# Kernel tuning notes

Measured on AMD Instinct MI355X. Metric: run time of the kernel, lower is better.

The kernel has to match this reference:

```python
import jax, jax.numpy as jnp
import numpy as np

NUM_LAYERS = 3
DROPOUT_P = 0.1


def _spmm(rows, cols, vals, X, num_rows):
    # COO SpMM: out[r] = sum_{e: rows[e]==r} vals[e] * X[cols[e]]
    return jax.ops.segment_sum(vals[:, None] * X[cols], rows, num_segments=num_rows)


def setup_inputs() -> dict:
    key = jax.random.key(0)
    ks = jax.random.split(key, 8)
    N, H, D, NNZ = 50000, 50000, 256, 1600000
    poi_embs = jax.random.normal(ks[0], (N, D), dtype=jnp.float32)
    src_row = jax.random.randint(ks[1], (NNZ,), 0, N, dtype=jnp.int32)
    src_col = jax.random.randint(ks[2], (NNZ,), 0, H, dtype=jnp.int32)
    src_val = jax.random.uniform(ks[3], (NNZ,), dtype=jnp.float32)
    tar_row = jax.random.randint(ks[4], (NNZ,), 0, H, dtype=jnp.int32)
    tar_col = jax.random.randint(ks[5], (NNZ,), 0, N, dtype=jnp.int32)
    tar_val = jax.random.uniform(ks[6], (NNZ,), dtype=jnp.float32)
    return {
        "poi_embs": poi_embs,
        "src_row": src_row, "src_col": src_col, "src_val": src_val,
        "tar_row": tar_row, "tar_col": tar_col, "tar_val": tar_val,
        "num_pois": N, "num_hyperedges": H,
    }


def reference(poi_embs, src_row, src_col, src_val, tar_row, tar_col, tar_val,
              num_pois, num_hyperedges):
    keep = 1.0 - DROPOUT_P
    drop_key = jax.random.key(42)
    finals = [poi_embs]  # [N, D]
    x = poi_embs
    for i in range(NUM_LAYERS):
        msg_tar = _spmm(tar_row, tar_col, tar_val, x, num_hyperedges)   # [H, D]
        msg_src = _spmm(src_row, src_col, src_val, msg_tar, num_pois)   # [N, D]
        h = msg_src + finals[-1]
        mask = jax.random.bernoulli(jax.random.fold_in(drop_key, i), keep, h.shape)
        x = jnp.where(mask, h / keep, 0.0)  # inverted dropout, training=True
        finals.append(x)
    return jnp.mean(jnp.stack(finals), axis=0)
```

## Files before the change

kernel.cpp:

```cpp
#include <hip/hip_runtime.h>
#include <hip/hip_fp16.h>
#include <stdint.h>

#define DD 256
#define BK_SHIFT 10
#define NB 98
#define CHUNK 4096

typedef float    fx4 __attribute__((ext_vector_type(4)));
typedef uint32_t ux2 __attribute__((ext_vector_type(2)));

__host__ __device__ __forceinline__ uint32_t rotl32(uint32_t v, int r) {
  return (v << r) | (v >> (32 - r));
}

__host__ __device__ inline void tf2x32(uint32_t k0, uint32_t k1,
                                       uint32_t& x0, uint32_t& x1) {
  uint32_t ks0 = k0, ks1 = k1, ks2 = k0 ^ k1 ^ 0x1BD11BDAu;
  x0 += ks0; x1 += ks1;
#define TF_RND(r) { x0 += x1; x1 = rotl32(x1, (r)); x1 ^= x0; }
  TF_RND(13) TF_RND(15) TF_RND(26) TF_RND(6)
  x0 += ks1; x1 += ks2 + 1u;
  TF_RND(17) TF_RND(29) TF_RND(16) TF_RND(24)
  x0 += ks2; x1 += ks0 + 2u;
  TF_RND(13) TF_RND(15) TF_RND(26) TF_RND(6)
  x0 += ks0; x1 += ks1 + 3u;
  TF_RND(17) TF_RND(29) TF_RND(16) TF_RND(24)
  x0 += ks1; x1 += ks2 + 4u;
  TF_RND(13) TF_RND(15) TF_RND(26) TF_RND(6)
  x0 += ks2; x1 += ks0 + 5u;
#undef TF_RND
}

__device__ __forceinline__ float2 h2f(uint32_t u) {
  __half2 h = *(__half2*)&u;
  return __half22float2(h);
}

__global__ void init_kernel(const float* __restrict__ p, uint32_t* __restrict__ xh,
                            int total4) {
  int t4 = blockIdx.x * blockDim.x + threadIdx.x;
  if (t4 >= total4) return;
  fx4 v = __builtin_nontemporal_load((const fx4*)p + t4);
  __half2 h0 = __floats2half2_rn(v.x, v.y);
  __half2 h1 = __floats2half2_rn(v.z, v.w);
  ux2 u;
  u.x = *(const uint32_t*)&h0;
  u.y = *(const uint32_t*)&h1;
  __builtin_nontemporal_store(u, (ux2*)xh + t4);
}

__global__ __launch_bounds__(256) void bucket_hist(
    const int* __restrict__ t_row, int nnz_t,
    const int* __restrict__ s_row, int nnz_s,
    int* __restrict__ gbcnt, int H) {
  __shared__ int lcnt[NB];
  for (int i = threadIdx.x; i < NB; i += 256) lcnt[i] = 0;
  __syncthreads();
  const int base = blockIdx.x * CHUNK;
  const int nnz_all = nnz_t + nnz_s;
#pragma unroll
  for (int k = 0; k < CHUNK / 256; ++k) {
    int e = base + k * 256 + threadIdx.x;
    if (e < nnz_all) {
      int slot = (e < nnz_t) ? t_row[e] : (H + s_row[e - nnz_t]);
      atomicAdd(&lcnt[slot >> BK_SHIFT], 1);
    }
  }
  __syncthreads();
  for (int i = threadIdx.x; i < NB; i += 256)
    if (lcnt[i]) atomicAdd(&gbcnt[i], lcnt[i]);
}

__global__ void bucket_scan(const int* __restrict__ gbcnt,
                            int* __restrict__ bbase, int* __restrict__ gcur) {
  if (threadIdx.x == 0) {
    int run = 0;
    for (int i = 0; i < NB; ++i) { bbase[i] = run; gcur[i] = run; run += gbcnt[i]; }
    bbase[NB] = run;
  }
}

__global__ __launch_bounds__(256) void coarse_scatter(
    const int* __restrict__ t_row, const int* __restrict__ t_col,
    const float* __restrict__ t_val, int nnz_t,
    const int* __restrict__ s_row, const int* __restrict__ s_col,
    const float* __restrict__ s_val, int nnz_s,
    int* __restrict__ gcur, uint64_t* __restrict__ staging, int H) {
  __shared__ int lcnt[NB], lbase[NB], gofs[NB];
  __shared__ int ltotal;
  __shared__ uint64_t stage[CHUNK];
  const int tid = threadIdx.x;
  for (int i = tid; i < NB; i += 256) lcnt[i] = 0;
  __syncthreads();
  const int base = blockIdx.x * CHUNK;
  const int nnz_all = nnz_t + nnz_s;
  uint64_t rec[CHUNK / 256];
#pragma unroll
  for (int k = 0; k < CHUNK / 256; ++k) {
    int e = base + k * 256 + tid;
    if (e < nnz_all) {
      int slot, col; float val;
      if (e < nnz_t) { slot = t_row[e]; col = t_col[e]; val = t_val[e]; }
      else { int i2 = e - nnz_t; slot = H + s_row[i2]; col = s_col[i2]; val = s_val[i2]; }
      uint32_t packed = ((uint32_t)col << 16) |
                        (uint32_t)__half_as_ushort(__float2half_rn(val));
      rec[k] = ((uint64_t)(uint32_t)slot << 32) | packed;
      atomicAdd(&lcnt[slot >> BK_SHIFT], 1);
    } else {
      rec[k] = ~0ull;
    }
  }
  __syncthreads();
  if (tid == 0) {
    int run = 0;
    for (int i = 0; i < NB; ++i) { lbase[i] = run; run += lcnt[i]; }
    ltotal = run;
  }
  __syncthreads();
  if (tid < NB) {
    if (lcnt[tid]) gofs[tid] = atomicAdd(&gcur[tid], lcnt[tid]);
    lcnt[tid] = 0;
  }
  __syncthreads();
#pragma unroll
  for (int k = 0; k < CHUNK / 256; ++k) {
    int slot = (int)(rec[k] >> 32);
    if (slot >= 0) {
      int b = slot >> BK_SHIFT;
      int p = atomicAdd(&lcnt[b], 1);
      stage[lbase[b] + p] = rec[k];
    }
  }
  __syncthreads();
  const int tot = ltotal;
  for (int i = tid; i < tot; i += 256) {
    uint64_t r = stage[i];
    int b = (int)(r >> 32) >> BK_SHIFT;
    staging[(size_t)gofs[b] + (i - lbase[b])] = r;
  }
}

__global__ __launch_bounds__(256) void fine_scatter(
    const uint64_t* __restrict__ staging, const int* __restrict__ bbase,
    int* __restrict__ offs, uint32_t* __restrict__ epk, int slots) {
  __shared__ int scnt[1024];
  __shared__ int sofs[1024];
  __shared__ int wsum[4];
  const int b = blockIdx.x;
  const int bb = bbase[b], be = bbase[b + 1];
  const int tid = threadIdx.x;
  for (int i = tid; i < 1024; i += 256) scnt[i] = 0;
  __syncthreads();
  for (int i = bb + tid; i < be; i += 256)
    atomicAdd(&scnt[(int)(staging[i] >> 32) & 1023], 1);
  __syncthreads();
  const int base4 = tid * 4;
  int v[4], pre[4];
#pragma unroll
  for (int k = 0; k < 4; ++k) v[k] = scnt[base4 + k];
  int tsum = 0;
#pragma unroll
  for (int k = 0; k < 4; ++k) { pre[k] = tsum; tsum += v[k]; }
  int lane = tid & 63, wv = tid >> 6;
  int inc = tsum;
  for (int off = 1; off < 64; off <<= 1) {
    int up = __shfl_up(inc, off, 64);
    if (lane >= off) inc += up;
  }
  if (lane == 63) wsum[wv] = inc;
  __syncthreads();
  int wbase = 0;
  for (int w = 0; w < wv; ++w) wbase += wsum[w];
  int texc = wbase + inc - tsum;
#pragma unroll
  for (int k = 0; k < 4; ++k) sofs[base4 + k] = texc + pre[k];
  __syncthreads();
#pragma unroll
  for (int k = 0; k < 4; ++k) {
    int g = (b << BK_SHIFT) + base4 + k;
    if (g < slots) offs[g] = bb + sofs[base4 + k] + v[k];
  }
  __syncthreads();
  for (int i = bb + tid; i < be; i += 256) {
    uint64_t r = staging[i];
    int ls = (int)(r >> 32) & 1023;
    int p = atomicAdd(&sofs[ls], 1);
    epk[(size_t)bb + p] = (uint32_t)r;
  }
}

#define GATHER_BODY(SRC)                                                          \
  float4 acc = make_float4(0.f, 0.f, 0.f, 0.f);                                   \
  int i = b;                                                                      \
  for (; i + 7 < e; i += 8) {                                                     \
    uint32_t E[8]; uint2 A[8];                                                    \
    _Pragma("unroll")                                                             \
    for (int k = 0; k < 8; ++k) E[k] = __builtin_nontemporal_load(ep + i + k);    \
    _Pragma("unroll")                                                             \
    for (int k = 0; k < 8; ++k) A[k] = SRC[(size_t)(E[k] >> 16) * 64 + lane];     \
    _Pragma("unroll")                                                             \
    for (int k = 0; k < 8; ++k) {                                                 \
      float v = __half2float(__ushort_as_half((unsigned short)(E[k] & 0xFFFFu))); \
      float2 f0 = h2f(A[k].x), f1 = h2f(A[k].y);                                  \
      acc.x += v * f0.x; acc.y += v * f0.y;                                       \
      acc.z += v * f1.x; acc.w += v * f1.y;                                       \
    }                                                                             \
  }                                                                               \
  for (; i < e; ++i) {                                                            \
    uint32_t E0 = __builtin_nontemporal_load(ep + i);                             \
    uint2 A0 = SRC[(size_t)(E0 >> 16) * 64 + lane];                               \
    float v = __half2float(__ushort_as_half((unsigned short)(E0 & 0xFFFFu)));     \
    float2 f0 = h2f(A0.x), f1 = h2f(A0.y);                                        \
    acc.x += v * f0.x; acc.y += v * f0.y;                                         \
    acc.z += v * f1.x; acc.w += v * f1.y;                                         \
  }

__global__ __launch_bounds__(256) void spmm_full(
    const int* __restrict__ offs, const uint32_t* __restrict__ ep,
    const uint2* __restrict__ X, uint2* __restrict__ Y, int nrows, int grow_base) {
  int wid = threadIdx.x >> 6, lane = threadIdx.x & 63;
  int r = blockIdx.x * 4 + wid;
  if (r >= nrows) return;
  int g = grow_base + r;
  int b = (g == 0) ? 0 : offs[g - 1];
  int e = offs[g];
  GATHER_BODY(X)
  __half2 o0 = __floats2half2_rn(acc.x, acc.y);
  __half2 o1 = __floats2half2_rn(acc.z, acc.w);
  uint2 o;
  o.x = *(const uint32_t*)&o0;
  o.y = *(const uint32_t*)&o1;
  Y[(size_t)r * 64 + lane] = o;
}

__global__ __launch_bounds__(256) void spmm_drop(
    const int* __restrict__ offs, const uint32_t* __restrict__ ep,
    const uint2* __restrict__ T, const uint2* __restrict__ xprev,
    uint2* __restrict__ xout, uint32_t k0, uint32_t k1, int nrows, int grow_base) {
  int wid = threadIdx.x >> 6, lane = threadIdx.x & 63;
  int r = blockIdx.x * 4 + wid;
  if (r >= nrows) return;
  int g = grow_base + r;
  int b = (g == 0) ? 0 : offs[g - 1];
  int e = offs[g];
  GATHER_BODY(T)
  size_t xi = (size_t)r * 64 + lane;
  ux2 xv_u = __builtin_nontemporal_load((const ux2*)xprev + xi);
  float2 x0f = h2f(xv_u.x), x1f = h2f(xv_u.y);
  float h[4] = {acc.x + x0f.x, acc.y + x0f.y, acc.z + x1f.x, acc.w + x1f.y};
  int j0 = r * DD + lane * 4;
  float xn[4];
#pragma unroll
  for (int k = 0; k < 4; ++k) {
    uint32_t r0 = 0u, r1 = (uint32_t)(j0 + k);
    tf2x32(k0, k1, r0, r1);
    uint32_t bits = r0 ^ r1;
    float u = __uint_as_float((bits >> 9) | 0x3f800000u) - 1.0f;
    xn[k] = (u < 0.9f) ? h[k] * (1.0f / 0.9f) : 0.0f;
  }
  __half2 nx0 = __floats2half2_rn(xn[0], xn[1]);
  __half2 nx1 = __floats2half2_rn(xn[2], xn[3]);
  ux2 nxu;
  nxu.x = *(const uint32_t*)&nx0;
  nxu.y = *(const uint32_t*)&nx1;
  __builtin_nontemporal_store(nxu, (ux2*)xout + xi);
}

__global__ __launch_bounds__(256) void spmm_drop_final(
    const int* __restrict__ offs, const uint32_t* __restrict__ ep,
    const uint2* __restrict__ T, const uint2* __restrict__ x0,
    const uint2* __restrict__ x1, const uint2* __restrict__ x2,
    float* __restrict__ out, uint32_t k0, uint32_t k1, int nrows, int grow_base) {
  int wid = threadIdx.x >> 6, lane = threadIdx.x & 63;
  int r = blockIdx.x * 4 + wid;
  if (r >= nrows) return;
  int g = grow_base + r;
  int b = (g == 0) ? 0 : offs[g - 1];
  int e = offs[g];
  GATHER_BODY(T)
  size_t xi = (size_t)r * 64 + lane;
  ux2 x2u = __builtin_nontemporal_load((const ux2*)x2 + xi);
  float2 q0 = h2f(x2u.x), q1 = h2f(x2u.y);
  float h[4] = {acc.x + q0.x, acc.y + q0.y, acc.z + q1.x, acc.w + q1.y};
  int j0 = r * DD + lane * 4;
  float xn[4];
#pragma unroll
  for (int k = 0; k < 4; ++k) {
    uint32_t r0 = 0u, r1 = (uint32_t)(j0 + k);
    tf2x32(k0, k1, r0, r1);
    uint32_t bits = r0 ^ r1;
    float u = __uint_as_float((bits >> 9) | 0x3f800000u) - 1.0f;
    xn[k] = (u < 0.9f) ? h[k] * (1.0f / 0.9f) : 0.0f;
  }
  ux2 x0u = __builtin_nontemporal_load((const ux2*)x0 + xi);
  ux2 x1u = __builtin_nontemporal_load((const ux2*)x1 + xi);
  float2 p0 = h2f(x0u.x), p1 = h2f(x0u.y);
  float2 a0 = h2f(x1u.x), a1 = h2f(x1u.y);
  fx4 ov;
  ov.x = 0.25f * (p0.x + a0.x + q0.x + xn[0]);
  ov.y = 0.25f * (p0.y + a0.y + q0.y + xn[1]);
  ov.z = 0.25f * (p1.x + a1.x + q1.x + xn[2]);
  ov.w = 0.25f * (p1.y + a1.y + q1.y + xn[3]);
  __builtin_nontemporal_store(ov, (fx4*)out + xi);
}

extern "C" void kernel_launch(void* const* d_in, const int* in_sizes, int n_in,
                              void* d_out, int out_size, void* d_ws, size_t ws_size,
                              hipStream_t stream) {
  const float* p     = (const float*)d_in[0];
  const int*   s_row = (const int*)d_in[1];
  const int*   s_col = (const int*)d_in[2];
  const float* s_val = (const float*)d_in[3];
  const int*   t_row = (const int*)d_in[4];
  const int*   t_col = (const int*)d_in[5];
  const float* t_val = (const float*)d_in[6];

  const int nnz_s = in_sizes[1];
  const int nnz_t = in_sizes[4];
  const int N = in_sizes[0] / DD;
  const int H = 50000;
  const int slots = H + N;
  const int nnz_all = nnz_t + nnz_s;

  uint2*    x0      = (uint2*)d_ws;
  uint2*    x1      = x0 + (size_t)N * 64;
  uint2*    th      = x1 + (size_t)N * 64;
  uint64_t* staging = (uint64_t*)(th + (size_t)H * 64);
  uint2*    x2      = (uint2*)staging;
  uint32_t* epk     = (uint32_t*)(staging + nnz_all);
  int*      offs    = (int*)(epk + nnz_all);
  int*      gbcnt   = offs + slots;
  int*      bbase   = gbcnt + NB;
  int*      gcur    = bbase + (NB + 1);

  float* out = (float*)d_out;

  (void)hipMemsetAsync(gbcnt, 0, sizeof(int) * NB, stream);
  const int cblocks = (nnz_all + CHUNK - 1) / CHUNK;
  bucket_hist<<<cblocks, 256, 0, stream>>>(t_row, nnz_t, s_row, nnz_s, gbcnt, H);
  bucket_scan<<<1, 64, 0, stream>>>(gbcnt, bbase, gcur);
  coarse_scatter<<<cblocks, 256, 0, stream>>>(t_row, t_col, t_val, nnz_t,
                                              s_row, s_col, s_val, nnz_s,
                                              gcur, staging, H);
  fine_scatter<<<NB, 256, 0, stream>>>(staging, bbase, offs, epk, slots);

  const int total4 = N * DD / 4;
  init_kernel<<<(total4 + 255) / 256, 256, 0, stream>>>(p, (uint32_t*)x0, total4);

  uint32_t key[3][2];
  for (int i = 0; i < 3; ++i) {
    uint32_t a = 0u, b = (uint32_t)i;
    tf2x32(0u, 42u, a, b);
    key[i][0] = a; key[i][1] = b;
  }

  spmm_full<<<(H + 3) / 4, 256, 0, stream>>>(offs, epk, x0, th, H, 0);
  spmm_drop<<<(N + 3) / 4, 256, 0, stream>>>(offs, epk, th, x0, x1,
                                             key[0][0], key[0][1], N, H);
  spmm_full<<<(H + 3) / 4, 256, 0, stream>>>(offs, epk, x1, th, H, 0);
  spmm_drop<<<(N + 3) / 4, 256, 0, stream>>>(offs, epk, th, x1, x2,
                                             key[1][0], key[1][1], N, H);
  spmm_full<<<(H + 3) / 4, 256, 0, stream>>>(offs, epk, x2, th, H, 0);
  spmm_drop_final<<<(N + 3) / 4, 256, 0, stream>>>(offs, epk, th, x0, x1, x2, out,
                                                   key[2][0], key[2][1], N, H);
}
```

Baseline: 815.1 us.

## Replace bucket histogram pass with fixed-slack bucket regions; unroll gather by 16

```diff
diff --git a/kernel.cpp b/kernel.cpp
--- a/kernel.cpp
+++ b/kernel.cpp
@@ -4,7 +4,9 @@
 
 #define DD 256
 #define BK_SHIFT 10
+#define BK_MASK 1023
 #define NB 98
+#define SLACK 40960
 #define CHUNK 4096
 
 typedef float    fx4 __attribute__((ext_vector_type(4)));
@@ -50,35 +52,9 @@
   __builtin_nontemporal_store(u, (ux2*)xh + t4);
 }
 
-__global__ __launch_bounds__(256) void bucket_hist(
-    const int* __restrict__ t_row, int nnz_t,
-    const int* __restrict__ s_row, int nnz_s,
-    int* __restrict__ gbcnt, int H) {
-  __shared__ int lcnt[NB];
-  for (int i = threadIdx.x; i < NB; i += 256) lcnt[i] = 0;
-  __syncthreads();
-  const int base = blockIdx.x * CHUNK;
-  const int nnz_all = nnz_t + nnz_s;
-#pragma unroll
-  for (int k = 0; k < CHUNK / 256; ++k) {
-    int e = base + k * 256 + threadIdx.x;
-    if (e < nnz_all) {
-      int slot = (e < nnz_t) ? t_row[e] : (H + s_row[e - nnz_t]);
-      atomicAdd(&lcnt[slot >> BK_SHIFT], 1);
-    }
-  }
-  __syncthreads();
-  for (int i = threadIdx.x; i < NB; i += 256)
-    if (lcnt[i]) atomicAdd(&gbcnt[i], lcnt[i]);
-}
-
-__global__ void bucket_scan(const int* __restrict__ gbcnt,
-                            int* __restrict__ bbase, int* __restrict__ gcur) {
-  if (threadIdx.x == 0) {
-    int run = 0;
-    for (int i = 0; i < NB; ++i) { bbase[i] = run; gcur[i] = run; run += gbcnt[i]; }
-    bbase[NB] = run;
-  }
+__global__ void gcur_init(int* __restrict__ gcur) {
+  int i = blockIdx.x * blockDim.x + threadIdx.x;
+  if (i < NB) gcur[i] = i * SLACK;
 }
 
 __global__ __launch_bounds__(256) void coarse_scatter(
@@ -142,18 +118,19 @@
 }
 
 __global__ __launch_bounds__(256) void fine_scatter(
-    const uint64_t* __restrict__ staging, const int* __restrict__ bbase,
+    const uint64_t* __restrict__ staging, const int* __restrict__ gcur,
     int* __restrict__ offs, uint32_t* __restrict__ epk, int slots) {
   __shared__ int scnt[1024];
   __shared__ int sofs[1024];
   __shared__ int wsum[4];
   const int b = blockIdx.x;
-  const int bb = bbase[b], be = bbase[b + 1];
+  const int bb = b * SLACK;
+  const int be = gcur[b];
   const int tid = threadIdx.x;
   for (int i = tid; i < 1024; i += 256) scnt[i] = 0;
   __syncthreads();
   for (int i = bb + tid; i < be; i += 256)
-    atomicAdd(&scnt[(int)(staging[i] >> 32) & 1023], 1);
+    atomicAdd(&scnt[(int)(staging[i] >> 32) & BK_MASK], 1);
   __syncthreads();
   const int base4 = tid * 4;
   int v[4], pre[4];
@@ -184,37 +161,46 @@
   __syncthreads();
   for (int i = bb + tid; i < be; i += 256) {
     uint64_t r = staging[i];
-    int ls = (int)(r >> 32) & 1023;
+    int ls = (int)(r >> 32) & BK_MASK;
     int p = atomicAdd(&sofs[ls], 1);
     epk[(size_t)bb + p] = (uint32_t)r;
   }
 }
 
-#define GATHER_BODY(SRC)                                                          \
-  float4 acc = make_float4(0.f, 0.f, 0.f, 0.f);                                   \
-  int i = b;                                                                      \
-  for (; i + 7 < e; i += 8) {                                                     \
-    uint32_t E[8]; uint2 A[8];                                                    \
+#define GB_STEP(NN)                                                               \
+  for (; i + (NN - 1) < e; i += NN) {                                             \
+    uint32_t E[NN]; uint2 A[NN];                                                  \
     _Pragma("unroll")                                                             \
-    for (int k = 0; k < 8; ++k) E[k] = __builtin_nontemporal_load(ep + i + k);    \
+    for (int k = 0; k < NN; ++k) E[k] = __builtin_nontemporal_load(ep + i + k);   \
     _Pragma("unroll")                                                             \
-    for (int k = 0; k < 8; ++k) A[k] = SRC[(size_t)(E[k] >> 16) * 64 + lane];     \
+    for (int k = 0; k < NN; ++k) A[k] = SRC_PTR[(size_t)(E[k] >> 16) * 64 + lane];\
     _Pragma("unroll")                                                             \
-    for (int k = 0; k < 8; ++k) {                                                 \
+    for (int k = 0; k < NN; ++k) {                                                \
       float v = __half2float(__ushort_as_half((unsigned short)(E[k] & 0xFFFFu))); \
       float2 f0 = h2f(A[k].x), f1 = h2f(A[k].y);                                  \
       acc.x += v * f0.x; acc.y += v * f0.y;                                       \
       acc.z += v * f1.x; acc.w += v * f1.y;                                       \
     }                                                                             \
-  }                                                                               \
+  }
+
+#define GATHER_BODY(SRC)                                                          \
+  float4 acc = make_float4(0.f, 0.f, 0.f, 0.f);                                   \
+  const uint2* SRC_PTR = (SRC);                                                   \
+  int i = b;                                                                      \
+  GB_STEP(16)                                                                     \
+  GB_STEP(8)                                                                      \
   for (; i < e; ++i) {                                                            \
     uint32_t E0 = __builtin_nontemporal_load(ep + i);                             \
-    uint2 A0 = SRC[(size_t)(E0 >> 16) * 64 + lane];                               \
+    uint2 A0 = SRC_PTR[(size_t)(E0 >> 16) * 64 + lane];                           \
     float v = __half2float(__ushort_as_half((unsigned short)(E0 & 0xFFFFu)));     \
     float2 f0 = h2f(A0.x), f1 = h2f(A0.y);                                        \
     acc.x += v * f0.x; acc.y += v * f0.y;                                         \
     acc.z += v * f1.x; acc.w += v * f1.y;                                         \
   }
+
+#define ROW_BOUNDS(G)                                                             \
+  int b = ((G) & BK_MASK) ? offs[(G) - 1] : ((G) >> BK_SHIFT) * SLACK;            \
+  int e = offs[(G)];
 
 __global__ __launch_bounds__(256) void spmm_full(
     const int* __restrict__ offs, const uint32_t* __restrict__ ep,
@@ -223,8 +209,7 @@
   int r = blockIdx.x * 4 + wid;
   if (r >= nrows) return;
   int g = grow_base + r;
-  int b = (g == 0) ? 0 : offs[g - 1];
-  int e = offs[g];
+  ROW_BOUNDS(g)
   GATHER_BODY(X)
   __half2 o0 = __floats2half2_rn(acc.x, acc.y);
   __half2 o1 = __floats2half2_rn(acc.z, acc.w);
@@ -242,8 +227,7 @@
   int r = blockIdx.x * 4 + wid;
   if (r >= nrows) return;
   int g = grow_base + r;
-  int b = (g == 0) ? 0 : offs[g - 1];
-  int e = offs[g];
+  ROW_BOUNDS(g)
   GATHER_BODY(T)
   size_t xi = (size_t)r * 64 + lane;
   ux2 xv_u = __builtin_nontemporal_load((const ux2*)xprev + xi);
@@ -276,8 +260,7 @@
   int r = blockIdx.x * 4 + wid;
   if (r >= nrows) return;
   int g = grow_base + r;
-  int b = (g == 0) ? 0 : offs[g - 1];
-  int e = offs[g];
+  ROW_BOUNDS(g)
   GATHER_BODY(T)
   size_t xi = (size_t)r * 64 + lane;
   ux2 x2u = __builtin_nontemporal_load((const ux2*)x2 + xi);
@@ -324,26 +307,22 @@
   const int nnz_all = nnz_t + nnz_s;
 
   uint2*    x0      = (uint2*)d_ws;
-  uint2*    x1      = x0 + (size_t)N * 64;
-  uint2*    th      = x1 + (size_t)N * 64;
-  uint64_t* staging = (uint64_t*)(th + (size_t)H * 64);
-  uint2*    x2      = (uint2*)staging;
-  uint32_t* epk     = (uint32_t*)(staging + nnz_all);
-  int*      offs    = (int*)(epk + nnz_all);
-  int*      gbcnt   = offs + slots;
-  int*      bbase   = gbcnt + NB;
-  int*      gcur    = bbase + (NB + 1);
+  uint2*    th      = x0 + (size_t)N * 64;
+  uint2*    x1      = th + (size_t)H * 64;
+  uint2*    x2      = x1 + (size_t)N * 64;
+  uint64_t* staging = (uint64_t*)x1;
+  uint32_t* epk     = (uint32_t*)(x2 + (size_t)N * 64);
+  int*      offs    = (int*)(epk + (size_t)NB * SLACK);
+  int*      gcur    = offs + slots;
 
   float* out = (float*)d_out;
 
-  (void)hipMemsetAsync(gbcnt, 0, sizeof(int) * NB, stream);
+  gcur_init<<<1, 128, 0, stream>>>(gcur);
   const int cblocks = (nnz_all + CHUNK - 1) / CHUNK;
-  bucket_hist<<<cblocks, 256, 0, stream>>>(t_row, nnz_t, s_row, nnz_s, gbcnt, H);
-  bucket_scan<<<1, 64, 0, stream>>>(gbcnt, bbase, gcur);
   coarse_scatter<<<cblocks, 256, 0, stream>>>(t_row, t_col, t_val, nnz_t,
                                               s_row, s_col, s_val, nnz_s,
                                               gcur, staging, H);
-  fine_scatter<<<NB, 256, 0, stream>>>(staging, bbase, offs, epk, slots);
+  fine_scatter<<<NB, 256, 0, stream>>>(staging, gcur, offs, epk, slots);
 
   const int total4 = N * DD / 4;
   init_kernel<<<(total4 + 255) / 256, 256, 0, stream>>>(p, (uint32_t*)x0, total4);
```

Measured after the change: 787.6 us. 3.4% less time.
